# Kernel optimization log

Hardware: AMD Instinct MI355X
Metric: run time of the kernel (lower is better)

## Reference

```python
import jax, jax.numpy as jnp
import numpy as np

D_MODEL = 1024
N_HEADS = 16
B, S = 4, 2048
SCALE = float(np.sqrt(D_MODEL))  # NOTE: source scales by sqrt(d_key)=sqrt(full dim), not sqrt(head dim)


def setup_inputs() -> dict:
    key = jax.random.key(0)
    ks = jax.random.split(key, 6)
    inv = 1.0 / np.sqrt(D_MODEL)
    return {
        "query": jax.random.normal(ks[0], (B, S, D_MODEL), dtype=jnp.float32),
        "key": jax.random.normal(ks[1], (B, S, D_MODEL), dtype=jnp.float32),
        "value": jax.random.normal(ks[2], (B, S, D_MODEL), dtype=jnp.float32),
        # torch Linear weights: [out_features, in_features], y = x @ W.T
        "wq": jax.random.uniform(ks[3], (D_MODEL, D_MODEL), jnp.float32, -inv, inv),
        "wk": jax.random.uniform(ks[4], (D_MODEL, D_MODEL), jnp.float32, -inv, inv),
        "wv": jax.random.uniform(ks[5], (D_MODEL, D_MODEL), jnp.float32, -inv, inv),
    }


def reference(query, key, value, wq, wk, wv):
    dh = D_MODEL // N_HEADS
    b, sq, _ = query.shape
    sk = key.shape[1]
    # projections (bias=False): x @ W.T
    q = (query @ wq.T).reshape(b, sq, N_HEADS, dh)
    k = (key @ wk.T).reshape(b, sk, N_HEADS, dh)
    v = (value @ wv.T).reshape(b, sk, N_HEADS, dh)
    # per-head scores; chunk(-1) == contiguous head split, same as reshape
    scores = jnp.einsum("bqhd,bkhd->bhqk", q, k) / SCALE
    probs = jax.nn.softmax(scores, axis=-1)
    out = jnp.einsum("bhqk,bkhd->bqhd", probs, v)
    return out.reshape(b, sq, D_MODEL)
```

## Files before the change

### kernel.cpp

```cpp
#include <hip/hip_runtime.h>
#include <hip/hip_bf16.h>
#include <stdint.h>

typedef __bf16 bf16;
typedef __attribute__((ext_vector_type(8))) __bf16 bf16x8;
typedef __attribute__((ext_vector_type(4))) __bf16 bf16x4;
typedef __attribute__((ext_vector_type(4))) float f32x4;

#define S_LEN 2048
#define DMODEL 1024
#define NH 16
#define BATCH 4

#define NX 8388608u
#define NW 1048576u
#define WC_OFF (3u * NX)
#define PP_OFF (WC_OFF + 3u * NW)

static __device__ __forceinline__ void gload_lds16(const void* g, void* l) {
  __builtin_amdgcn_global_load_lds(
      (const __attribute__((address_space(1))) void*)(g),
      (__attribute__((address_space(3))) void*)(l), 16, 0, 0);
}

struct CvtArgs {
  const float* s[6];
  bf16* d[6];
  int n[6];
};

__global__ __launch_bounds__(256) void cvt_f32_bf16(CvtArgs a) {
  const int ai = blockIdx.y;
  const float* __restrict__ s = a.s[ai];
  bf16* __restrict__ d = a.d[ai];
  const int n = a.n[ai];
  const int i = (blockIdx.x * 256 + threadIdx.x) * 8;
  if (i >= n) return;
  const float4* sp = reinterpret_cast<const float4*>(s + i);
  float4 x = sp[0];
  float4 y = sp[1];
  bf16x8 o;
  o[0] = (bf16)x.x; o[1] = (bf16)x.y; o[2] = (bf16)x.z; o[3] = (bf16)x.w;
  o[4] = (bf16)y.x; o[5] = (bf16)y.y; o[6] = (bf16)y.z; o[7] = (bf16)y.w;
  *reinterpret_cast<bf16x8*>(d + i) = o;
}

__global__ __launch_bounds__(256, 2) void proj_gemm(const bf16* __restrict__ Xc,
                                                    const bf16* __restrict__ Wc,
                                                    bf16* __restrict__ Yp) {
  const int z = blockIdx.z;
  const bf16* __restrict__ X = Xc + (size_t)z * NX;
  const bf16* __restrict__ W = Wc + (size_t)z * NW;
  bf16* __restrict__ Y = Yp + (size_t)z * NX;

  __shared__ bf16 ldsA[128 * 32];
  __shared__ bf16 ldsB[128 * 32];

  const int tid = threadIdx.x;
  const int lane = tid & 63;
  const int w = tid >> 6;
  const int wr = w >> 1, wc = w & 1;
  const int r16 = lane & 15, g4 = lane >> 4;
  const int m0 = blockIdx.x * 128, n0 = blockIdx.y * 128;

  f32x4 acc[4][4];
#pragma unroll
  for (int mi = 0; mi < 4; mi++)
#pragma unroll
    for (int ni = 0; ni < 4; ni++)
      acc[mi][ni] = (f32x4){0.f, 0.f, 0.f, 0.f};

  const int rowa = tid >> 2;
  const int cola = (tid & 3) * 8;

  for (int k0 = 0; k0 < DMODEL; k0 += 32) {
    gload_lds16(X + (size_t)(m0 + rowa) * DMODEL + k0 + cola, &ldsA[tid * 8]);
    gload_lds16(X + (size_t)(m0 + 64 + rowa) * DMODEL + k0 + cola, &ldsA[2048 + tid * 8]);
    gload_lds16(W + (size_t)(n0 + rowa) * DMODEL + k0 + cola, &ldsB[tid * 8]);
    gload_lds16(W + (size_t)(n0 + 64 + rowa) * DMODEL + k0 + cola, &ldsB[2048 + tid * 8]);
    __syncthreads();

    bf16x8 af[4], bfr[4];
#pragma unroll
    for (int mi = 0; mi < 4; mi++)
      af[mi] = *reinterpret_cast<const bf16x8*>(
          &ldsA[(wr * 64 + mi * 16 + r16) * 32 + g4 * 8]);
#pragma unroll
    for (int ni = 0; ni < 4; ni++)
      bfr[ni] = *reinterpret_cast<const bf16x8*>(
          &ldsB[(wc * 64 + ni * 16 + r16) * 32 + g4 * 8]);
#pragma unroll
    for (int mi = 0; mi < 4; mi++)
#pragma unroll
      for (int ni = 0; ni < 4; ni++)
        acc[mi][ni] = __builtin_amdgcn_mfma_f32_16x16x32_bf16(
            af[mi], bfr[ni], acc[mi][ni], 0, 0, 0);
    __syncthreads();
  }

#pragma unroll
  for (int mi = 0; mi < 4; mi++)
#pragma unroll
    for (int ni = 0; ni < 4; ni++)
#pragma unroll
      for (int i = 0; i < 4; i++) {
        const int row = m0 + wr * 64 + mi * 16 + g4 * 4 + i;
        const int col = n0 + wc * 64 + ni * 16 + r16;
        Y[(size_t)row * DMODEL + col] = (bf16)acc[mi][ni][i];
      }
}

__global__ __launch_bounds__(256, 2) void attn_kernel(const bf16* __restrict__ Qp,
                                                      const bf16* __restrict__ Kp,
                                                      const bf16* __restrict__ Vp,
                                                      float* __restrict__ Out) {
  __shared__ bf16 ldsK[64 * 64];
  __shared__ bf16 ldsVt[64 * 64];
  __shared__ bf16 ldsP[4][32 * 64];

  const int tid = threadIdx.x;
  const int lane = tid & 63;
  const int w = tid >> 6;
  const int r16 = lane & 15, g4 = lane >> 4;
  const int b = blockIdx.z, h = blockIdx.y;
  const int q0 = blockIdx.x * 128 + w * 32;

  bf16x8 qf[2][2];
#pragma unroll
  for (int qi = 0; qi < 2; qi++)
#pragma unroll
    for (int kk = 0; kk < 2; kk++)
      qf[qi][kk] = *reinterpret_cast<const bf16x8*>(
          Qp + (size_t)(b * S_LEN + q0 + qi * 16 + r16) * DMODEL + h * 64 +
          kk * 32 + g4 * 8);

  f32x4 oacc[2][4];
#pragma unroll
  for (int mi = 0; mi < 2; mi++)
#pragma unroll
    for (int nd = 0; nd < 4; nd++)
      oacc[mi][nd] = (f32x4){0.f, 0.f, 0.f, 0.f};

  float mrun[2] = {-1e30f, -1e30f};
  float lrun[2] = {0.f, 0.f};
  const float inv_scale = 1.0f / 32.0f;

  const int srow = tid >> 3;
  const int scol = (tid & 7) * 8;
  const int kswz = ((tid >> 3) & 7) * 8;
  const int vxor = (tid & 7) * 8;

  for (int it = 0; it < S_LEN / 64; it++) {
    const int kv0 = it * 64;
    gload_lds16(Kp + (size_t)(b * S_LEN + kv0 + srow) * DMODEL + h * 64 + (scol ^ kswz),
                &ldsK[tid * 8]);
    gload_lds16(Kp + (size_t)(b * S_LEN + kv0 + 32 + srow) * DMODEL + h * 64 + (scol ^ kswz),
                &ldsK[2048 + tid * 8]);
#pragma unroll
    for (int half = 0; half < 2; half++) {
      const int rv = srow + half * 32;
      bf16x8 v = *reinterpret_cast<const bf16x8*>(
          Vp + (size_t)(b * S_LEN + kv0 + rv) * DMODEL + h * 64 + scol);
      const int rsw = rv ^ vxor;
#pragma unroll
      for (int j = 0; j < 8; j++) ldsVt[(scol + j) * 64 + rsw] = v[j];
    }
    __syncthreads();

    f32x4 sacc[4][2];
#pragma unroll
    for (int kvi = 0; kvi < 4; kvi++)
#pragma unroll
      for (int qi = 0; qi < 2; qi++) sacc[kvi][qi] = (f32x4){0.f, 0.f, 0.f, 0.f};
#pragma unroll
    for (int kk = 0; kk < 2; kk++) {
      bf16x8 kf[4];
#pragma unroll
      for (int kvi = 0; kvi < 4; kvi++) {
        const int kvr = kvi * 16 + r16;
        const int c = (kk * 32 + g4 * 8) ^ ((kvr & 7) * 8);
        kf[kvi] = *reinterpret_cast<const bf16x8*>(&ldsK[kvr * 64 + c]);
      }
#pragma unroll
      for (int kvi = 0; kvi < 4; kvi++)
#pragma unroll
        for (int qi = 0; qi < 2; qi++)
          sacc[kvi][qi] = __builtin_amdgcn_mfma_f32_16x16x32_bf16(
              kf[kvi], qf[qi][kk], sacc[kvi][qi], 0, 0, 0);
    }

#pragma unroll
    for (int qi = 0; qi < 2; qi++) {
      float tmax = -1e30f;
#pragma unroll
      for (int kvi = 0; kvi < 4; kvi++)
#pragma unroll
        for (int i = 0; i < 4; i++) tmax = fmaxf(tmax, sacc[kvi][qi][i]);
      tmax = fmaxf(tmax, __shfl_xor(tmax, 16, 64));
      tmax = fmaxf(tmax, __shfl_xor(tmax, 32, 64));
      const float mnew = fmaxf(mrun[qi], tmax * inv_scale);
      const float corr = __expf(mrun[qi] - mnew);
      float psum = 0.f;
      const int q = qi * 16 + r16;
#pragma unroll
      for (int kvi = 0; kvi < 4; kvi++) {
        float p0 = __expf(fmaf(sacc[kvi][qi][0], inv_scale, -mnew));
        float p1 = __expf(fmaf(sacc[kvi][qi][1], inv_scale, -mnew));
        float p2 = __expf(fmaf(sacc[kvi][qi][2], inv_scale, -mnew));
        float p3 = __expf(fmaf(sacc[kvi][qi][3], inv_scale, -mnew));
        psum += (p0 + p1) + (p2 + p3);
        const int kvbase = (kvi * 16 + g4 * 4) ^ ((q & 7) * 8);
        bf16x4 pk;
        pk[0] = (bf16)p0; pk[1] = (bf16)p1; pk[2] = (bf16)p2; pk[3] = (bf16)p3;
        *reinterpret_cast<bf16x4*>(&ldsP[w][q * 64 + kvbase]) = pk;
      }
      psum += __shfl_xor(psum, 16, 64);
      psum += __shfl_xor(psum, 32, 64);
      lrun[qi] = lrun[qi] * corr + psum;
      mrun[qi] = mnew;
#pragma unroll
      for (int i = 0; i < 4; i++) {
        const float corr_r = __shfl(corr, g4 * 4 + i, 64);
#pragma unroll
        for (int nd = 0; nd < 4; nd++) oacc[qi][nd][i] *= corr_r;
      }
    }

#pragma unroll
    for (int kk = 0; kk < 2; kk++) {
      bf16x8 pf[2], vf[4];
#pragma unroll
      for (int mi = 0; mi < 2; mi++) {
        const int q = mi * 16 + r16;
        const int c = (kk * 32 + g4 * 8) ^ ((q & 7) * 8);
        pf[mi] = *reinterpret_cast<const bf16x8*>(&ldsP[w][q * 64 + c]);
      }
#pragma unroll
      for (int nd = 0; nd < 4; nd++) {
        const int d = nd * 16 + r16;
        const int c = (kk * 32 + g4 * 8) ^ (((d >> 3) & 7) * 8);
        vf[nd] = *reinterpret_cast<const bf16x8*>(&ldsVt[d * 64 + c]);
      }
#pragma unroll
      for (int mi = 0; mi < 2; mi++)
#pragma unroll
        for (int nd = 0; nd < 4; nd++)
          oacc[mi][nd] = __builtin_amdgcn_mfma_f32_16x16x32_bf16(
              pf[mi], vf[nd], oacc[mi][nd], 0, 0, 0);
    }
    __syncthreads();
  }

#pragma unroll
  for (int mi = 0; mi < 2; mi++)
#pragma unroll
    for (int i = 0; i < 4; i++) {
      const float lr = __shfl(lrun[mi], g4 * 4 + i, 64);
      const float inv_l = 1.0f / lr;
      const int q = q0 + mi * 16 + g4 * 4 + i;
#pragma unroll
      for (int nd = 0; nd < 4; nd++)
        Out[(size_t)(b * S_LEN + q) * DMODEL + h * 64 + nd * 16 + r16] =
            oacc[mi][nd][i] * inv_l;
    }
}

extern "C" void kernel_launch(void* const* d_in, const int* in_sizes, int n_in,
                              void* d_out, int out_size, void* d_ws, size_t ws_size,
                              hipStream_t stream) {
  const float* q = (const float*)d_in[0];
  const float* k = (const float*)d_in[1];
  const float* v = (const float*)d_in[2];
  const float* wq = (const float*)d_in[3];
  const float* wk = (const float*)d_in[4];
  const float* wv = (const float*)d_in[5];
  bf16* ws = (bf16*)d_ws;
  bf16* Xc = ws;
  bf16* Wc = ws + WC_OFF;
  bf16* Pp = ws + PP_OFF;
  float* out = (float*)d_out;

  CvtArgs ca;
  ca.s[0] = q;  ca.s[1] = k;  ca.s[2] = v;
  ca.s[3] = wq; ca.s[4] = wk; ca.s[5] = wv;
  ca.d[0] = Xc;          ca.d[1] = Xc + NX;     ca.d[2] = Xc + 2 * NX;
  ca.d[3] = Wc;          ca.d[4] = Wc + NW;     ca.d[5] = Wc + 2 * NW;
  ca.n[0] = ca.n[1] = ca.n[2] = (int)NX;
  ca.n[3] = ca.n[4] = ca.n[5] = (int)NW;
  cvt_f32_bf16<<<dim3(4096, 6, 1), dim3(256), 0, stream>>>(ca);

  proj_gemm<<<dim3(64, 8, 3), dim3(256), 0, stream>>>(Xc, Wc, Pp);

  attn_kernel<<<dim3(S_LEN / 128, NH, BATCH), dim3(256), 0, stream>>>(
      Pp, Pp + NX, Pp + 2 * NX, out);
}
```

Before: 358.6 us.

## Double-buffer LDS in projection and attention, add lazy rescale and exp2 softmax

Both the projection GEMM and the attention kernel now double-buffer their LDS tiles, so global loads for the next K/V or k-slice are issued before the current tile's MFMAs and overlap with them. The attention softmax switches to exp2 with a prefolded log2e/scale constant, and it skips the running-max rescale unless the new max exceeds the old one by a threshold. The GEMM epilogue stages results through LDS so stores are vectorized, MFMA sections get setprio, the V-transpose swizzle is changed, and the occupancy hint is raised to 3. The extra LDS for double buffers may limit the occupancy that was requested.

```diff
diff --git a/kernel.cpp b/kernel.cpp
--- a/kernel.cpp
+++ b/kernel.cpp
@@ -21,6 +21,10 @@
   __builtin_amdgcn_global_load_lds(
       (const __attribute__((address_space(1))) void*)(g),
       (__attribute__((address_space(3))) void*)(l), 16, 0, 0);
+}
+
+static __device__ __forceinline__ void wait_lds() {
+  asm volatile("s_waitcnt lgkmcnt(0)" ::: "memory");
 }
 
 struct CvtArgs {
@@ -45,7 +49,7 @@
   *reinterpret_cast<bf16x8*>(d + i) = o;
 }
 
-__global__ __launch_bounds__(256, 2) void proj_gemm(const bf16* __restrict__ Xc,
+__global__ __launch_bounds__(256, 3) void proj_gemm(const bf16* __restrict__ Xc,
                                                     const bf16* __restrict__ Wc,
                                                     bf16* __restrict__ Yp) {
   const int z = blockIdx.z;
@@ -53,8 +57,8 @@
   const bf16* __restrict__ W = Wc + (size_t)z * NW;
   bf16* __restrict__ Y = Yp + (size_t)z * NX;
 
-  __shared__ bf16 ldsA[128 * 32];
-  __shared__ bf16 ldsB[128 * 32];
+  __shared__ bf16 ldsA[2][128 * 32];
+  __shared__ bf16 ldsB[2][128 * 32];
 
   const int tid = threadIdx.x;
   const int lane = tid & 63;
@@ -67,55 +71,81 @@
 #pragma unroll
   for (int mi = 0; mi < 4; mi++)
 #pragma unroll
-    for (int ni = 0; ni < 4; ni++)
-      acc[mi][ni] = (f32x4){0.f, 0.f, 0.f, 0.f};
+    for (int ni = 0; ni < 4; ni++) acc[mi][ni] = (f32x4){0.f, 0.f, 0.f, 0.f};
 
   const int rowa = tid >> 2;
   const int cola = (tid & 3) * 8;
 
+  auto stage = [&](int buf, int k0) {
+    gload_lds16(X + (size_t)(m0 + rowa) * DMODEL + k0 + cola, &ldsA[buf][tid * 8]);
+    gload_lds16(X + (size_t)(m0 + 64 + rowa) * DMODEL + k0 + cola,
+                &ldsA[buf][2048 + tid * 8]);
+    gload_lds16(W + (size_t)(n0 + rowa) * DMODEL + k0 + cola, &ldsB[buf][tid * 8]);
+    gload_lds16(W + (size_t)(n0 + 64 + rowa) * DMODEL + k0 + cola,
+                &ldsB[buf][2048 + tid * 8]);
+  };
+
+  stage(0, 0);
+  __syncthreads();
+  int cur = 0;
+
   for (int k0 = 0; k0 < DMODEL; k0 += 32) {
-    gload_lds16(X + (size_t)(m0 + rowa) * DMODEL + k0 + cola, &ldsA[tid * 8]);
-    gload_lds16(X + (size_t)(m0 + 64 + rowa) * DMODEL + k0 + cola, &ldsA[2048 + tid * 8]);
-    gload_lds16(W + (size_t)(n0 + rowa) * DMODEL + k0 + cola, &ldsB[tid * 8]);
-    gload_lds16(W + (size_t)(n0 + 64 + rowa) * DMODEL + k0 + cola, &ldsB[2048 + tid * 8]);
-    __syncthreads();
+    if (k0 + 32 < DMODEL) stage(cur ^ 1, k0 + 32);
 
     bf16x8 af[4], bfr[4];
 #pragma unroll
     for (int mi = 0; mi < 4; mi++)
       af[mi] = *reinterpret_cast<const bf16x8*>(
-          &ldsA[(wr * 64 + mi * 16 + r16) * 32 + g4 * 8]);
+          &ldsA[cur][(wr * 64 + mi * 16 + r16) * 32 + g4 * 8]);
 #pragma unroll
     for (int ni = 0; ni < 4; ni++)
       bfr[ni] = *reinterpret_cast<const bf16x8*>(
-          &ldsB[(wc * 64 + ni * 16 + r16) * 32 + g4 * 8]);
+          &ldsB[cur][(wc * 64 + ni * 16 + r16) * 32 + g4 * 8]);
+    __builtin_amdgcn_s_setprio(1);
 #pragma unroll
     for (int mi = 0; mi < 4; mi++)
 #pragma unroll
       for (int ni = 0; ni < 4; ni++)
         acc[mi][ni] = __builtin_amdgcn_mfma_f32_16x16x32_bf16(
             af[mi], bfr[ni], acc[mi][ni], 0, 0, 0);
+    __builtin_amdgcn_s_setprio(0);
     __syncthreads();
+    cur ^= 1;
   }
 
-#pragma unroll
-  for (int mi = 0; mi < 4; mi++)
+  float* shf = reinterpret_cast<float*>(&ldsA[0][0]) + w * 1024;
+#pragma unroll
+  for (int mi = 0; mi < 4; mi++) {
 #pragma unroll
     for (int ni = 0; ni < 4; ni++)
 #pragma unroll
       for (int i = 0; i < 4; i++) {
-        const int row = m0 + wr * 64 + mi * 16 + g4 * 4 + i;
-        const int col = n0 + wc * 64 + ni * 16 + r16;
-        Y[(size_t)row * DMODEL + col] = (bf16)acc[mi][ni][i];
-      }
-}
-
-__global__ __launch_bounds__(256, 2) void attn_kernel(const bf16* __restrict__ Qp,
+        const int rl = g4 * 4 + i;
+        const int cl = ni * 16 + r16;
+        shf[rl * 64 + ((cl + 4 * rl) & 63)] = acc[mi][ni][i];
+      }
+    wait_lds();
+#pragma unroll
+    for (int cc = 0; cc < 4; cc++) {
+      const int row = g4 + cc * 4;
+      const int c0 = r16 * 4;
+      const f32x4 vv = *reinterpret_cast<const f32x4*>(
+          &shf[row * 64 + ((c0 + 4 * row) & 63)]);
+      bf16x4 o;
+      o[0] = (bf16)vv[0]; o[1] = (bf16)vv[1]; o[2] = (bf16)vv[2]; o[3] = (bf16)vv[3];
+      *reinterpret_cast<bf16x4*>(
+          Y + (size_t)(m0 + wr * 64 + mi * 16 + row) * DMODEL + n0 + wc * 64 + c0) = o;
+    }
+    wait_lds();
+  }
+}
+
+__global__ __launch_bounds__(256, 3) void attn_kernel(const bf16* __restrict__ Qp,
                                                       const bf16* __restrict__ Kp,
                                                       const bf16* __restrict__ Vp,
                                                       float* __restrict__ Out) {
-  __shared__ bf16 ldsK[64 * 64];
-  __shared__ bf16 ldsVt[64 * 64];
+  __shared__ bf16 ldsK[2][64 * 64];
+  __shared__ bf16 ldsVt[2][64 * 64];
   __shared__ bf16 ldsP[4][32 * 64];
 
   const int tid = threadIdx.x;
@@ -138,34 +168,52 @@
 #pragma unroll
   for (int mi = 0; mi < 2; mi++)
 #pragma unroll
-    for (int nd = 0; nd < 4; nd++)
-      oacc[mi][nd] = (f32x4){0.f, 0.f, 0.f, 0.f};
+    for (int nd = 0; nd < 4; nd++) oacc[mi][nd] = (f32x4){0.f, 0.f, 0.f, 0.f};
 
   float mrun[2] = {-1e30f, -1e30f};
   float lrun[2] = {0.f, 0.f};
-  const float inv_scale = 1.0f / 32.0f;
+  const float C2 = 0.04508422002778011f;
 
   const int srow = tid >> 3;
   const int scol = (tid & 7) * 8;
-  const int kswz = ((tid >> 3) & 7) * 8;
-  const int vxor = (tid & 7) * 8;
-
-  for (int it = 0; it < S_LEN / 64; it++) {
-    const int kv0 = it * 64;
+  const int kswz = (srow & 7) * 8;
+
+  auto stageK = [&](int buf, int kv0) {
     gload_lds16(Kp + (size_t)(b * S_LEN + kv0 + srow) * DMODEL + h * 64 + (scol ^ kswz),
-                &ldsK[tid * 8]);
+                &ldsK[buf][tid * 8]);
     gload_lds16(Kp + (size_t)(b * S_LEN + kv0 + 32 + srow) * DMODEL + h * 64 + (scol ^ kswz),
-                &ldsK[2048 + tid * 8]);
-#pragma unroll
-    for (int half = 0; half < 2; half++) {
-      const int rv = srow + half * 32;
-      bf16x8 v = *reinterpret_cast<const bf16x8*>(
-          Vp + (size_t)(b * S_LEN + kv0 + rv) * DMODEL + h * 64 + scol);
-      const int rsw = rv ^ vxor;
-#pragma unroll
-      for (int j = 0; j < 8; j++) ldsVt[(scol + j) * 64 + rsw] = v[j];
-    }
-    __syncthreads();
+                &ldsK[buf][2048 + tid * 8]);
+  };
+  bf16x8 vpre0, vpre1;
+  auto loadV = [&](int kv0) {
+    vpre0 = *reinterpret_cast<const bf16x8*>(
+        Vp + (size_t)(b * S_LEN + kv0 + srow) * DMODEL + h * 64 + scol);
+    vpre1 = *reinterpret_cast<const bf16x8*>(
+        Vp + (size_t)(b * S_LEN + kv0 + 32 + srow) * DMODEL + h * 64 + scol);
+  };
+  auto writeV = [&](int buf) {
+#pragma unroll
+    for (int j = 0; j < 8; j++) {
+      const int d = scol + j;
+      const int vsw = (((scol >> 3) ^ j) & 7) * 8;
+      ldsVt[buf][d * 64 + (srow ^ vsw)] = vpre0[j];
+      ldsVt[buf][d * 64 + ((srow + 32) ^ vsw)] = vpre1[j];
+    }
+  };
+
+  stageK(0, 0);
+  loadV(0);
+  writeV(0);
+  __syncthreads();
+  int cur = 0;
+
+  constexpr int NT = S_LEN / 64;
+  for (int it = 0; it < NT; it++) {
+    const bool pf = (it + 1 < NT);
+    if (pf) {
+      stageK(cur ^ 1, (it + 1) * 64);
+      loadV((it + 1) * 64);
+    }
 
     f32x4 sacc[4][2];
 #pragma unroll
@@ -178,15 +226,17 @@
 #pragma unroll
       for (int kvi = 0; kvi < 4; kvi++) {
         const int kvr = kvi * 16 + r16;
-        const int c = (kk * 32 + g4 * 8) ^ ((kvr & 7) * 8);
-        kf[kvi] = *reinterpret_cast<const bf16x8*>(&ldsK[kvr * 64 + c]);
-      }
+        const int c = (kk * 32 + g4 * 8) ^ ((r16 & 7) * 8);
+        kf[kvi] = *reinterpret_cast<const bf16x8*>(&ldsK[cur][kvr * 64 + c]);
+      }
+      __builtin_amdgcn_s_setprio(1);
 #pragma unroll
       for (int kvi = 0; kvi < 4; kvi++)
 #pragma unroll
         for (int qi = 0; qi < 2; qi++)
           sacc[kvi][qi] = __builtin_amdgcn_mfma_f32_16x16x32_bf16(
               kf[kvi], qf[qi][kk], sacc[kvi][qi], 0, 0, 0);
+      __builtin_amdgcn_s_setprio(0);
     }
 
 #pragma unroll
@@ -198,16 +248,21 @@
         for (int i = 0; i < 4; i++) tmax = fmaxf(tmax, sacc[kvi][qi][i]);
       tmax = fmaxf(tmax, __shfl_xor(tmax, 16, 64));
       tmax = fmaxf(tmax, __shfl_xor(tmax, 32, 64));
-      const float mnew = fmaxf(mrun[qi], tmax * inv_scale);
-      const float corr = __expf(mrun[qi] - mnew);
+      const float tm2 = tmax * C2;
+      const bool resc = !__all(tm2 <= mrun[qi] + 11.0f);
+      float mnew = mrun[qi], corr = 1.f;
+      if (resc) {
+        mnew = fmaxf(mrun[qi], tm2);
+        corr = exp2f(mrun[qi] - mnew);
+      }
       float psum = 0.f;
       const int q = qi * 16 + r16;
 #pragma unroll
       for (int kvi = 0; kvi < 4; kvi++) {
-        float p0 = __expf(fmaf(sacc[kvi][qi][0], inv_scale, -mnew));
-        float p1 = __expf(fmaf(sacc[kvi][qi][1], inv_scale, -mnew));
-        float p2 = __expf(fmaf(sacc[kvi][qi][2], inv_scale, -mnew));
-        float p3 = __expf(fmaf(sacc[kvi][qi][3], inv_scale, -mnew));
+        float p0 = exp2f(fmaf(sacc[kvi][qi][0], C2, -mnew));
+        float p1 = exp2f(fmaf(sacc[kvi][qi][1], C2, -mnew));
+        float p2 = exp2f(fmaf(sacc[kvi][qi][2], C2, -mnew));
+        float p3 = exp2f(fmaf(sacc[kvi][qi][3], C2, -mnew));
         psum += (p0 + p1) + (p2 + p3);
         const int kvbase = (kvi * 16 + g4 * 4) ^ ((q & 7) * 8);
         bf16x4 pk;
@@ -216,39 +271,48 @@
       }
       psum += __shfl_xor(psum, 16, 64);
       psum += __shfl_xor(psum, 32, 64);
-      lrun[qi] = lrun[qi] * corr + psum;
-      mrun[qi] = mnew;
-#pragma unroll
-      for (int i = 0; i < 4; i++) {
-        const float corr_r = __shfl(corr, g4 * 4 + i, 64);
-#pragma unroll
-        for (int nd = 0; nd < 4; nd++) oacc[qi][nd][i] *= corr_r;
+      if (resc) {
+        lrun[qi] = lrun[qi] * corr + psum;
+        mrun[qi] = mnew;
+#pragma unroll
+        for (int i = 0; i < 4; i++) {
+          const float corr_r = __shfl(corr, g4 * 4 + i, 64);
+#pragma unroll
+          for (int nd = 0; nd < 4; nd++) oacc[qi][nd][i] *= corr_r;
+        }
+      } else {
+        lrun[qi] += psum;
       }
     }
 
 #pragma unroll
     for (int kk = 0; kk < 2; kk++) {
-      bf16x8 pf[2], vf[4];
+      bf16x8 pfg[2], vf[4];
 #pragma unroll
       for (int mi = 0; mi < 2; mi++) {
         const int q = mi * 16 + r16;
         const int c = (kk * 32 + g4 * 8) ^ ((q & 7) * 8);
-        pf[mi] = *reinterpret_cast<const bf16x8*>(&ldsP[w][q * 64 + c]);
+        pfg[mi] = *reinterpret_cast<const bf16x8*>(&ldsP[w][q * 64 + c]);
       }
 #pragma unroll
       for (int nd = 0; nd < 4; nd++) {
         const int d = nd * 16 + r16;
-        const int c = (kk * 32 + g4 * 8) ^ (((d >> 3) & 7) * 8);
-        vf[nd] = *reinterpret_cast<const bf16x8*>(&ldsVt[d * 64 + c]);
-      }
+        const int c = (kk * 32 + g4 * 8) ^ ((((d >> 3) ^ d) & 7) * 8);
+        vf[nd] = *reinterpret_cast<const bf16x8*>(&ldsVt[cur][d * 64 + c]);
+      }
+      __builtin_amdgcn_s_setprio(1);
 #pragma unroll
       for (int mi = 0; mi < 2; mi++)
 #pragma unroll
         for (int nd = 0; nd < 4; nd++)
           oacc[mi][nd] = __builtin_amdgcn_mfma_f32_16x16x32_bf16(
-              pf[mi], vf[nd], oacc[mi][nd], 0, 0, 0);
-    }
+              pfg[mi], vf[nd], oacc[mi][nd], 0, 0, 0);
+      __builtin_amdgcn_s_setprio(0);
+    }
+
+    if (pf) writeV(cur ^ 1);
     __syncthreads();
+    cur ^= 1;
   }
 
 #pragma unroll
```

New measurement: 353.5 us. About the same (-1.4%).
